# Kernel optimization log

Measured on AMD Instinct MI355X. Metric: run time of the kernel, lower is better.

The kernel has to match this reference:

```python
import jax, jax.numpy as jnp
import numpy as np

H = 501
T = 200
V = 71


def gru_layer(x, h0, W_ih, W_hh, b_ih, b_hh):
    # x: [B,T,I], h0: [B,H]; PyTorch GRU gate order: r, z, n
    gi = jnp.einsum('bti,gi->btg', x, W_ih) + b_ih  # [B,T,3H]

    def step(h, gi_t):
        gh = h @ W_hh.T + b_hh  # [B,3H]
        r = jax.nn.sigmoid(gi_t[:, :H] + gh[:, :H])
        z = jax.nn.sigmoid(gi_t[:, H:2 * H] + gh[:, H:2 * H])
        n = jnp.tanh(gi_t[:, 2 * H:] + r * gh[:, 2 * H:])
        h_new = (1.0 - z) * n + z * h
        return h_new, h_new

    h_last, ys = jax.lax.scan(step, h0, jnp.swapaxes(gi, 0, 1))
    return jnp.swapaxes(ys, 0, 1), h_last  # [B,T,H], [B,H]


def setup_inputs() -> dict:
    key = jax.random.key(0)
    ks = jax.random.split(key, 16)
    s = 1.0 / np.sqrt(H)
    u = lambda k, shp: jax.random.uniform(k, shp, jnp.float32, -s, s)
    return {
        'x': jax.random.normal(ks[0], (256, 1), jnp.float32),
        'W_ih1': u(ks[1], (3 * H, 1)), 'W_hh1': u(ks[2], (3 * H, H)),
        'b_ih1': u(ks[3], (3 * H,)), 'b_hh1': u(ks[4], (3 * H,)),
        'W_ih2': u(ks[5], (3 * H, H)), 'W_hh2': u(ks[6], (3 * H, H)),
        'b_ih2': u(ks[7], (3 * H,)), 'b_hh2': u(ks[8], (3 * H,)),
        'W_ih3': u(ks[9], (3 * H, H)), 'W_hh3': u(ks[10], (3 * H, H)),
        'b_ih3': u(ks[11], (3 * H,)), 'b_hh3': u(ks[12], (3 * H,)),
        'Wd': u(ks[13], (V, H)), 'bd': u(ks[14], (V,)),
    }


def reference(x, W_ih1, W_hh1, b_ih1, b_hh1, W_ih2, W_hh2, b_ih2, b_hh2,
              W_ih3, W_hh3, b_ih3, b_hh3, Wd, bd):
    B = x.shape[0]
    # repeat_vector: tile latent scalar across T timesteps -> [B,T,1]
    xr = jnp.broadcast_to(x[:, None, :], (B, T, 1))
    h0 = jnp.zeros((B, H), x.dtype)
    o1, h1 = gru_layer(xr, h0, W_ih1, W_hh1, b_ih1, b_hh1)
    o1 = jnp.tanh(o1)
    o2, h2 = gru_layer(o1, h1, W_ih2, W_hh2, b_ih2, b_hh2)
    o2 = jnp.tanh(o2)
    o3, _ = gru_layer(o2, h2, W_ih3, W_hh3, b_ih3, b_hh3)
    o3 = jnp.tanh(o3)
    logits = jax.nn.relu(jnp.einsum('bth,vh->btv', o3, Wd) + bd)  # [B,T,V]
    return logits
```

## Files before the change

kernel.cpp:

```cpp
#include <hip/hip_runtime.h>
#include <hip/hip_fp16.h>

typedef _Float16 half8 __attribute__((ext_vector_type(8)));
typedef float floatx16 __attribute__((ext_vector_type(16)));

#define HID 501
#define TT  200
#define BB  256
#define VV  71
#define HP  512

#define OFF_BAR   0ull
#define OFF_HFRAG 4096ull
#define SZ_HFRAG  (2ull*8*32*512*2)
#define OFF_HFIN  (OFF_HFRAG + SZ_HFRAG)
#define SZ_HFIN   (256ull*512*4)
#define OFF_GI1   (OFF_HFIN + SZ_HFIN)
#define SZ_GI1    (256ull*1536*4)
#define OFF_BIAS  (OFF_GI1 + SZ_GI1)
#define SZ_BIAS   (65536ull)
#define OFF_WD    (OFF_BIAS + SZ_BIAS)
#define SZ_WD     (96ull*512*2)
#define OFF_BD    (OFF_WD + SZ_WD)
#define SZ_BD     4096ull
#define OFF_W     (OFF_BD + SZ_BD)
#define SZ_W      (3ull*2*32*2*32*1024*2)
#define OFF_OFRAG (OFF_W + SZ_W)
#define SZ_OBUF   (8ull*200*32*512*2)
#define WS_NEED   (OFF_OFRAG + 2ull*SZ_OBUF)

#define COH_LD16(dst, p) \
  asm volatile("global_load_dwordx4 %0, %1, off sc0 sc1" : "=&v"(dst) : "v"(p) : "memory")
__device__ __forceinline__ void coh_store16(_Float16* p, half8 v) {
  asm volatile("global_store_dwordx4 %0, %1, off sc0 sc1" :: "v"(p), "v"(v) : "memory");
}
__device__ __forceinline__ void coh_st4(unsigned* p, unsigned v) {
  asm volatile("global_store_dword %0, %1, off sc0 sc1" :: "v"(p), "v"(v) : "memory");
}
__device__ __forceinline__ float tanh_fast(float x) {
  float e = __expf(2.f*x);
  return 1.f - 2.f/(e + 1.f);
}

__global__ __launch_bounds__(256) void prep_weights(
    const float* __restrict__ wih1, const float* __restrict__ whh1,
    const float* __restrict__ wih2, const float* __restrict__ whh2,
    const float* __restrict__ wih3, const float* __restrict__ whh3,
    _Float16* __restrict__ wbuf)
{
  const float* WIH[3] = {wih1, wih2, wih3};
  const float* WHH[3] = {whh1, whh2, whh3};
  const long total = 3ll << 21;
  for (long idx = (long)blockIdx.x*256 + threadIdx.x; idx < total; idx += (long)gridDim.x*256) {
    int k   = (int)(idx & 1023);
    int row = (int)((idx >> 10) & 31);
    int rt  = (int)((idx >> 15) & 1);
    int blk = (int)((idx >> 16) & 31);
    int L   = (int)(idx >> 21);
    int g, hl; bool ok;
    if (rt == 0) { g = row >> 4; hl = row & 15; ok = true; }
    else         { g = 2;        hl = row & 15; ok = (row < 16); }
    int hcol = blk*16 + hl;
    ok = ok && (hcol < HID);
    float w = 0.f;
    if (ok) {
      if (k < HP) { if (L > 0 && k < HID) w = WIH[L][(g*HID + hcol)*HID + k]; }
      else        { int kk = k - HP; if (kk < HID) w = WHH[L][(g*HID + hcol)*HID + kk]; }
    }
    _Float16 wh = (_Float16)w;
    _Float16 wl = (_Float16)(w - (float)wh);
    long oh = ((((long)(L*2+0)*32 + blk)*2 + rt)*32 + row)*1024 + k;
    long ol = ((((long)(L*2+1)*32 + blk)*2 + rt)*32 + row)*1024 + k;
    wbuf[oh] = wh;
    wbuf[ol] = wl;
  }
}

__global__ __launch_bounds__(256) void prep_misc(
    const float* __restrict__ x, const float* __restrict__ wih1,
    const float* __restrict__ bih1, const float* __restrict__ bhh1,
    const float* __restrict__ bih2, const float* __restrict__ bhh2,
    const float* __restrict__ bih3, const float* __restrict__ bhh3,
    const float* __restrict__ wd, const float* __restrict__ bd,
    float* __restrict__ gi1, float* __restrict__ bias,
    _Float16* __restrict__ wdbuf, float* __restrict__ bdbuf)
{
  const int N1 = 256*1536;
  const int N2 = 3*2*1536;
  const int N3 = 96*512;
  const int N4 = 96;
  for (int idx = blockIdx.x*256 + threadIdx.x; idx < N1+N2+N3+N4; idx += gridDim.x*256) {
    if (idx < N1) {
      int b = idx / 1536, m = idx % 1536;
      int g = m >> 9, hc = m & 511;
      float v = 0.f;
      if (hc < HID) { int r = g*HID + hc; v = x[b]*wih1[r] + bih1[r]; }
      gi1[idx] = v;
    } else if (idx < N1+N2) {
      int i2 = idx - N1;
      int L = i2 / (2*1536);
      int rest = i2 % (2*1536);
      int pl = rest / 1536, m = rest % 1536;
      int g = m >> 9, hc = m & 511;
      float v = 0.f;
      if (hc < HID) {
        int r = g*HID + hc;
        if (pl == 0) v = (L==0) ? 0.f : (L==1 ? bih2[r] : bih3[r]);
        else         v = (L==0) ? bhh1[r] : (L==1 ? bhh2[r] : bhh3[r]);
      }
      bias[i2] = v;
    } else if (idx < N1+N2+N3) {
      int i3 = idx - (N1+N2);
      int v = i3 >> 9, k = i3 & 511;
      float val = (v < VV && k < HID) ? wd[v*HID + k] : 0.f;
      wdbuf[i3] = (_Float16)val;
    } else {
      int v = idx - (N1+N2+N3);
      bdbuf[v] = (v < VV) ? bd[v] : 0.f;
    }
  }
}

template<int L>
__global__ __launch_bounds__(512, 1) void gru_layer_k(
    const _Float16* __restrict__ wbuf,
    const _Float16* __restrict__ osrc,
    _Float16* __restrict__ odst,
    _Float16* __restrict__ hfrag,
    float* __restrict__ hfin,
    const float* __restrict__ gi1,
    const float* __restrict__ bias,
    unsigned* __restrict__ flags)
{
  constexpr int KPW = (L==0) ? 4 : 8;
  const int bid  = blockIdx.x;
  const int tile = bid & 7;
  const int sl   = bid >> 3;
  const int tid  = threadIdx.x;
  const int w    = tid >> 6;
  const int lane = tid & 63;

  __shared__ float    ldsC[8][2][32][32];
  __shared__ _Float16 ldsH[2][32][16];
  __shared__ unsigned ldsFlag;

  if (tid == 0)
    __hip_atomic_store(&ldsFlag, 0u, __ATOMIC_RELAXED, __HIP_MEMORY_SCOPE_WORKGROUP);

  half8 Wf[2][2][KPW];
  {
    int row = lane & 31;
    int kc  = (lane >> 5) << 3;
    int ks0 = (L==0) ? (32 + w*4) : (w*8);
    #pragma unroll
    for (int pl = 0; pl < 2; ++pl)
      #pragma unroll
      for (int rt = 0; rt < 2; ++rt)
        #pragma unroll
        for (int i = 0; i < KPW; ++i) {
          long off = ((((long)(L*2+pl)*32 + sl)*2 + rt)*32 + row)*1024 + (long)(ks0+i)*16 + kc;
          Wf[pl][rt][i] = *(const half8*)(wbuf + off);
        }
  }

  const int b     = tid & 31;
  const int hl    = (tid >> 5) & 15;
  const int bglob = tile*32 + b;
  const int hglob = sl*16 + hl;
  float hreg = 0.f;
  float bih[3], bhh[3], gi[3] = {0,0,0};
  if (L > 0) hreg = hfin[bglob*HP + hglob];
  #pragma unroll
  for (int g = 0; g < 3; ++g) {
    bih[g] = bias[(L*2+0)*1536 + g*512 + hglob];
    bhh[g] = bias[(L*2+1)*1536 + g*512 + hglob];
    if (L == 0) gi[g] = gi1[(long)bglob*1536 + g*512 + hglob];
  }

  const long hf_par  = 8ll*32*512;
  const long hf_tile = (long)tile*(32*512);
  const long ob_t    = (long)tile*200*(32*512);
  const long region  = (long)sl*512;
  unsigned* fl = flags + tile*32;
  unsigned dead = 0;

  for (int t = 0; t < TT; ++t) {
    if (L > 0 && w < 4) {
      const _Float16* xb = osrc + ob_t + (long)t*(32*512) + (long)(w*8)*512 + lane*8;
      half8 X[8];
      #pragma unroll
      for (int i = 0; i < 8; ++i) X[i] = *(const half8*)(xb + i*512);
      floatx16 C0, C1;
      #pragma unroll
      for (int i = 0; i < 16; ++i) { C0[i] = 0.f; C1[i] = 0.f; }
      #pragma unroll
      for (int i = 0; i < 8; ++i) {
        C0 = __builtin_amdgcn_mfma_f32_32x32x16_f16(Wf[0][0][i], X[i], C0, 0, 0, 0);
        C0 = __builtin_amdgcn_mfma_f32_32x32x16_f16(Wf[1][0][i], X[i], C0, 0, 0, 0);
        C1 = __builtin_amdgcn_mfma_f32_32x32x16_f16(Wf[0][1][i], X[i], C1, 0, 0, 0);
        C1 = __builtin_amdgcn_mfma_f32_32x32x16_f16(Wf[1][1][i], X[i], C1, 0, 0, 0);
      }
      int col = lane & 31, rb = (lane >> 5) << 2;
      #pragma unroll
      for (int r = 0; r < 16; ++r) {
        int rowm = (r & 3) + 8*(r >> 2) + rb;
        ldsC[w][0][rowm][col] = C0[r];
        ldsC[w][1][rowm][col] = C1[r];
      }
    }
    if ((L == 0 || w >= 4) && !(L == 0 && t == 0)) {
      if (t > 0 && w != 5) {
        unsigned tries = 0;
        while (__hip_atomic_load(&ldsFlag, __ATOMIC_ACQUIRE,
                                 __HIP_MEMORY_SCOPE_WORKGROUP) < (unsigned)t) {
          if (++tries > (1u<<18)) { dead = 1; break; }
        }
        __builtin_amdgcn_sched_barrier(0);
      }
      const int hs0 = (L==0) ? (w*4) : ((w-4)*8);
      const _Float16* hp = hfrag + (long)(t & 1)*hf_par + hf_tile + (long)hs0*512 + lane*8;
      half8 H[KPW];
      #pragma unroll
      for (int i = 0; i < KPW; ++i) COH_LD16(H[i], hp + i*512);
      asm volatile("s_waitcnt vmcnt(0)" ::: "memory");
      __builtin_amdgcn_sched_barrier(0);
      floatx16 C0, C1;
      #pragma unroll
      for (int i = 0; i < 16; ++i) { C0[i] = 0.f; C1[i] = 0.f; }
      #pragma unroll
      for (int i = 0; i < KPW; ++i) {
        C0 = __builtin_amdgcn_mfma_f32_32x32x16_f16(Wf[0][0][i], H[i], C0, 0, 0, 0);
        C0 = __builtin_amdgcn_mfma_f32_32x32x16_f16(Wf[1][0][i], H[i], C0, 0, 0, 0);
        C1 = __builtin_amdgcn_mfma_f32_32x32x16_f16(Wf[0][1][i], H[i], C1, 0, 0, 0);
        C1 = __builtin_amdgcn_mfma_f32_32x32x16_f16(Wf[1][1][i], H[i], C1, 0, 0, 0);
      }
      int col = lane & 31, rb = (lane >> 5) << 2;
      #pragma unroll
      for (int r = 0; r < 16; ++r) {
        int rowm = (r & 3) + 8*(r >> 2) + rb;
        ldsC[w][0][rowm][col] = C0[r];
        ldsC[w][1][rowm][col] = C1[r];
      }
    }
    __syncthreads();
    {
      float sx[3] = {0,0,0}, sh[3] = {0,0,0};
      if (!(L == 0 && t == 0)) {
        #pragma unroll
        for (int g = 0; g < 3; ++g) {
          int rt  = (g == 2) ? 1 : 0;
          int row = (g == 2) ? hl : g*16 + hl;
          float ax = 0.f, ah = 0.f;
          if (L == 0) {
            #pragma unroll
            for (int ww = 0; ww < 8; ++ww) ah += ldsC[ww][rt][row][b];
          } else {
            #pragma unroll
            for (int ww = 0; ww < 4; ++ww) ax += ldsC[ww][rt][row][b];
            #pragma unroll
            for (int ww = 4; ww < 8; ++ww) ah += ldsC[ww][rt][row][b];
          }
          sx[g] = ax; sh[g] = ah;
        }
      }
      float pr = sx[0] + gi[0] + bih[0] + sh[0] + bhh[0];
      float pz = sx[1] + gi[1] + bih[1] + sh[1] + bhh[1];
      float r = 1.f/(1.f + __expf(-pr));
      float z = 1.f/(1.f + __expf(-pz));
      float n = tanh_fast(sx[2] + gi[2] + bih[2] + r*(sh[2] + bhh[2]));
      float hn = (1.f - z)*n + z*hreg;
      hreg = hn;
      ldsH[0][b][hl] = (_Float16)hn;
      ldsH[1][b][hl] = (_Float16)tanh_fast(hn);
      if (t == TT-1) hfin[bglob*HP + hglob] = hn;
    }
    __syncthreads();
    if (tid < 64) {
      int h0 = (tid >> 5) * 8;
      half8 hv = *(const half8*)&ldsH[0][tid & 31][h0];
      coh_store16(hfrag + (long)((t+1) & 1)*hf_par + hf_tile + region + tid*8, hv);
    }
    if (w == 0) {
      asm volatile("s_waitcnt vmcnt(0)" ::: "memory");
      if (tid == 0 && t < TT-1)
        coh_st4(fl + sl, (unsigned)(L*(TT-1) + t + 1));
    }
    if (tid < 64) {
      int h0 = (tid >> 5) * 8;
      half8 ov = *(const half8*)&ldsH[1][tid & 31][h0];
      *(half8*)(odst + ob_t + (long)t*(32*512) + region + tid*8) = ov;
    }
    if (w == 5 && t < TT-1) {
      if (!dead) {
        const unsigned tgt = (unsigned)(L*(TT-1) + t + 1);
        const unsigned* fp = fl + (lane & 31);
        unsigned tries = 0;
        for (;;) {
          unsigned v0, v1, v2, v3;
          asm volatile(
            "global_load_dword %0, %4, off sc0 sc1\n\t"
            "global_load_dword %1, %4, off sc0 sc1\n\t"
            "global_load_dword %2, %4, off sc0 sc1\n\t"
            "global_load_dword %3, %4, off sc0 sc1"
            : "=&v"(v0), "=&v"(v1), "=&v"(v2), "=&v"(v3)
            : "v"(fp) : "memory");
          asm volatile("s_waitcnt vmcnt(3)" ::: "memory");
          __builtin_amdgcn_sched_barrier(0);
          if (__all(v0 >= tgt)) break;
          asm volatile("s_waitcnt vmcnt(2)" ::: "memory");
          __builtin_amdgcn_sched_barrier(0);
          if (__all(v1 >= tgt)) break;
          asm volatile("s_waitcnt vmcnt(1)" ::: "memory");
          __builtin_amdgcn_sched_barrier(0);
          if (__all(v2 >= tgt)) break;
          asm volatile("s_waitcnt vmcnt(0)" ::: "memory");
          __builtin_amdgcn_sched_barrier(0);
          if (__all(v3 >= tgt)) break;
          if (++tries > (1u<<17)) { dead = 1; break; }
        }
        asm volatile("s_waitcnt vmcnt(0)" ::: "memory");
      }
      if (lane == 0)
        __hip_atomic_store(&ldsFlag, (unsigned)(t + 1), __ATOMIC_RELEASE,
                           __HIP_MEMORY_SCOPE_WORKGROUP);
    }
  }
}

__global__ __launch_bounds__(256, 2) void decoder_k(
    const _Float16* __restrict__ o3,
    const _Float16* __restrict__ wdbuf,
    const float* __restrict__ bdbuf,
    float* __restrict__ out)
{
  const int bx = blockIdx.x;
  const int tile = bx & 7;
  const int chunk = bx >> 3;
  const int tid = threadIdx.x;
  const int w = tid >> 6, lane = tid & 63;
  __shared__ float ldsD[4][96][32];
  __shared__ float ldsO[32][73];

  half8 Wf[3][8];
  {
    int kc = (lane >> 5) << 3;
    #pragma unroll
    for (int mt = 0; mt < 3; ++mt)
      #pragma unroll
      for (int i = 0; i < 8; ++i) {
        int row = mt*32 + (lane & 31);
        int k = (w*8 + i)*16 + kc;
        Wf[mt][i] = *(const half8*)(wdbuf + (long)row*512 + k);
      }
  }
  for (int tt = 0; tt < 8; ++tt) {
    int t = chunk*8 + tt;
    long ob = ((long)tile*200 + t)*(32*512);
    half8 Xf[8];
    #pragma unroll
    for (int i = 0; i < 8; ++i) {
      int s = w*8 + i;
      Xf[i] = *(const half8*)(o3 + ob + (long)s*512 + lane*8);
    }
    floatx16 C0, C1, C2;
    #pragma unroll
    for (int i = 0; i < 16; ++i) { C0[i] = 0.f; C1[i] = 0.f; C2[i] = 0.f; }
    #pragma unroll
    for (int i = 0; i < 8; ++i) {
      C0 = __builtin_amdgcn_mfma_f32_32x32x16_f16(Wf[0][i], Xf[i], C0, 0, 0, 0);
      C1 = __builtin_amdgcn_mfma_f32_32x32x16_f16(Wf[1][i], Xf[i], C1, 0, 0, 0);
      C2 = __builtin_amdgcn_mfma_f32_32x32x16_f16(Wf[2][i], Xf[i], C2, 0, 0, 0);
    }
    {
      int col = lane & 31;
      int rb = (lane >> 5) << 2;
      #pragma unroll
      for (int r = 0; r < 16; ++r) {
        int rowm = (r & 3) + 8*(r >> 2) + rb;
        ldsD[w][rowm][col]      = C0[r];
        ldsD[w][32 + rowm][col] = C1[r];
        ldsD[w][64 + rowm][col] = C2[r];
      }
    }
    __syncthreads();
    for (int ii = tid; ii < VV*32; ii += 256) {
      int bb = ii & 31, v = ii >> 5;
      float s = ldsD[0][v][bb] + ldsD[1][v][bb] + ldsD[2][v][bb] + ldsD[3][v][bb] + bdbuf[v];
      ldsO[bb][v] = s > 0.f ? s : 0.f;
    }
    __syncthreads();
    for (int ii = tid; ii < VV*32; ii += 256) {
      int bb = ii / VV, v = ii - bb*VV;
      out[((long)(tile*32 + bb)*200 + t)*VV + v] = ldsO[bb][v];
    }
    __syncthreads();
  }
}

extern "C" void kernel_launch(void* const* d_in, const int* in_sizes, int n_in,
                              void* d_out, int out_size, void* d_ws, size_t ws_size,
                              hipStream_t stream) {
  (void)in_sizes; (void)n_in;
  const float* x    = (const float*)d_in[0];
  const float* wih1 = (const float*)d_in[1];
  const float* whh1 = (const float*)d_in[2];
  const float* bih1 = (const float*)d_in[3];
  const float* bhh1 = (const float*)d_in[4];
  const float* wih2 = (const float*)d_in[5];
  const float* whh2 = (const float*)d_in[6];
  const float* bih2 = (const float*)d_in[7];
  const float* bhh2 = (const float*)d_in[8];
  const float* wih3 = (const float*)d_in[9];
  const float* whh3 = (const float*)d_in[10];
  const float* bih3 = (const float*)d_in[11];
  const float* bhh3 = (const float*)d_in[12];
  const float* wd   = (const float*)d_in[13];
  const float* bd   = (const float*)d_in[14];
  char* ws = (char*)d_ws;

  if (ws_size < WS_NEED) {
    hipMemsetAsync(d_out, 0, (size_t)out_size*sizeof(float), stream);
    return;
  }

  _Float16* wbuf   = (_Float16*)(ws + OFF_W);
  float*    gi1p   = (float*)(ws + OFF_GI1);
  float*    biasp  = (float*)(ws + OFF_BIAS);
  _Float16* wdbufp = (_Float16*)(ws + OFF_WD);
  float*    bdbufp = (float*)(ws + OFF_BD);
  _Float16* hfragp = (_Float16*)(ws + OFF_HFRAG);
  float*    hfinp  = (float*)(ws + OFF_HFIN);
  unsigned* flagsp = (unsigned*)(ws + OFF_BAR);
  _Float16* ob0    = (_Float16*)(ws + OFF_OFRAG);
  _Float16* ob1    = ob0 + SZ_OBUF/2;

  hipMemsetAsync(ws + OFF_BAR, 0, 4096, stream);

  prep_weights<<<4096, 256, 0, stream>>>(wih1, whh1, wih2, whh2, wih3, whh3, wbuf);
  prep_misc<<<1024, 256, 0, stream>>>(x, wih1, bih1, bhh1, bih2, bhh2, bih3, bhh3,
                                      wd, bd, gi1p, biasp, wdbufp, bdbufp);

  gru_layer_k<0><<<256, 512, 0, stream>>>(wbuf, ob1, ob0, hfragp, hfinp, gi1p, biasp, flagsp);
  gru_layer_k<1><<<256, 512, 0, stream>>>(wbuf, ob0, ob1, hfragp, hfinp, gi1p, biasp, flagsp);
  gru_layer_k<2><<<256, 512, 0, stream>>>(wbuf, ob1, ob0, hfragp, hfinp, gi1p, biasp, flagsp);

  decoder_k<<<200, 256, 0, stream>>>(ob0, wdbufp, bdbufp, (float*)d_out);
}
```

Measured before the change: 1.908 ms.

## Merge h-fragment store, flag publish and poll into one wave per step

The hidden-state fragment store, the flag publish and the cross-block flag poll now all run on wave 5. The poll loads are issued before the own-flag store, and the block's own flag slot is skipped when checking. The tanh output store moves to wave 6. The aim is to shorten the critical path of the per-timestep inter-block barrier by removing the wave-0 vmcnt drain and overlapping the publish with the first poll. The risk is ordering: the flag store must become visible only after the h-fragment store, and here that depends on the vmcnt counting being correct.

After: 1.964 ms. 2.9% more time.

```diff
diff --git a/kernel.cpp b/kernel.cpp
--- a/kernel.cpp
+++ b/kernel.cpp
@@ -275,27 +275,21 @@
       if (t == TT-1) hfin[bglob*HP + hglob] = hn;
     }
     __syncthreads();
-    if (tid < 64) {
-      int h0 = (tid >> 5) * 8;
-      half8 hv = *(const half8*)&ldsH[0][tid & 31][h0];
-      coh_store16(hfrag + (long)((t+1) & 1)*hf_par + hf_tile + region + tid*8, hv);
-    }
-    if (w == 0) {
-      asm volatile("s_waitcnt vmcnt(0)" ::: "memory");
-      if (tid == 0 && t < TT-1)
-        coh_st4(fl + sl, (unsigned)(L*(TT-1) + t + 1));
-    }
-    if (tid < 64) {
-      int h0 = (tid >> 5) * 8;
-      half8 ov = *(const half8*)&ldsH[1][tid & 31][h0];
-      *(half8*)(odst + ob_t + (long)t*(32*512) + region + tid*8) = ov;
-    }
-    if (w == 5 && t < TT-1) {
-      if (!dead) {
+    if (w == 6) {
+      int h0 = (lane >> 5) * 8;
+      half8 ov = *(const half8*)&ldsH[1][lane & 31][h0];
+      *(half8*)(odst + ob_t + (long)t*(32*512) + region + lane*8) = ov;
+    }
+    if (w == 5) {
+      int h0 = (lane >> 5) * 8;
+      half8 hv = *(const half8*)&ldsH[0][lane & 31][h0];
+      coh_store16(hfrag + (long)((t+1) & 1)*hf_par + hf_tile + region + lane*8, hv);
+      if (t < TT-1) {
         const unsigned tgt = (unsigned)(L*(TT-1) + t + 1);
         const unsigned* fp = fl + (lane & 31);
-        unsigned tries = 0;
-        for (;;) {
+        const bool own = ((lane & 31) == sl);
+        bool okp = false;
+        if (!dead) {
           unsigned v0, v1, v2, v3;
           asm volatile(
             "global_load_dword %0, %4, off sc0 sc1\n\t"
@@ -304,25 +298,56 @@
             "global_load_dword %3, %4, off sc0 sc1"
             : "=&v"(v0), "=&v"(v1), "=&v"(v2), "=&v"(v3)
             : "v"(fp) : "memory");
-          asm volatile("s_waitcnt vmcnt(3)" ::: "memory");
+          asm volatile("s_waitcnt vmcnt(4)" ::: "memory");
           __builtin_amdgcn_sched_barrier(0);
-          if (__all(v0 >= tgt)) break;
-          asm volatile("s_waitcnt vmcnt(2)" ::: "memory");
+          if (lane == 0) coh_st4(fl + sl, tgt);
+          asm volatile("s_waitcnt vmcnt(4)" ::: "memory");
           __builtin_amdgcn_sched_barrier(0);
-          if (__all(v1 >= tgt)) break;
-          asm volatile("s_waitcnt vmcnt(1)" ::: "memory");
-          __builtin_amdgcn_sched_barrier(0);
-          if (__all(v2 >= tgt)) break;
+          okp = __all(own || v0 >= tgt);
+          if (!okp) {
+            asm volatile("s_waitcnt vmcnt(3)" ::: "memory");
+            __builtin_amdgcn_sched_barrier(0);
+            okp = __all(own || v1 >= tgt);
+          }
+          if (!okp) {
+            asm volatile("s_waitcnt vmcnt(2)" ::: "memory");
+            __builtin_amdgcn_sched_barrier(0);
+            okp = __all(own || v2 >= tgt);
+          }
+          if (!okp) {
+            asm volatile("s_waitcnt vmcnt(1)" ::: "memory");
+            __builtin_amdgcn_sched_barrier(0);
+            okp = __all(own || v3 >= tgt);
+          }
+          unsigned tries = 0;
+          while (!okp) {
+            asm volatile(
+              "global_load_dword %0, %4, off sc0 sc1\n\t"
+              "global_load_dword %1, %4, off sc0 sc1\n\t"
+              "global_load_dword %2, %4, off sc0 sc1\n\t"
+              "global_load_dword %3, %4, off sc0 sc1"
+              : "=&v"(v0), "=&v"(v1), "=&v"(v2), "=&v"(v3)
+              : "v"(fp) : "memory");
+            asm volatile("s_waitcnt vmcnt(3)" ::: "memory");
+            __builtin_amdgcn_sched_barrier(0);
+            if (__all(own || v0 >= tgt)) { okp = true; break; }
+            asm volatile("s_waitcnt vmcnt(2)" ::: "memory");
+            __builtin_amdgcn_sched_barrier(0);
+            if (__all(own || v1 >= tgt)) { okp = true; break; }
+            asm volatile("s_waitcnt vmcnt(1)" ::: "memory");
+            __builtin_amdgcn_sched_barrier(0);
+            if (__all(own || v2 >= tgt)) { okp = true; break; }
+            asm volatile("s_waitcnt vmcnt(0)" ::: "memory");
+            __builtin_amdgcn_sched_barrier(0);
+            if (__all(own || v3 >= tgt)) { okp = true; break; }
+            if (++tries > (1u<<17)) { dead = 1; break; }
+          }
           asm volatile("s_waitcnt vmcnt(0)" ::: "memory");
-          __builtin_amdgcn_sched_barrier(0);
-          if (__all(v3 >= tgt)) break;
-          if (++tries > (1u<<17)) { dead = 1; break; }
         }
-        asm volatile("s_waitcnt vmcnt(0)" ::: "memory");
-      }
-      if (lane == 0)
-        __hip_atomic_store(&ldsFlag, (unsigned)(t + 1), __ATOMIC_RELEASE,
-                           __HIP_MEMORY_SCOPE_WORKGROUP);
+        if (lane == 0)
+          __hip_atomic_store(&ldsFlag, (unsigned)(t + 1), __ATOMIC_RELEASE,
+                             __HIP_MEMORY_SCOPE_WORKGROUP);
+      }
     }
   }
 }
```
